# Performance work log

Measured on AMD Instinct MI355X. Metric: run time of the kernel, lower is better.

The kernel has to match this reference:

```python
import jax, jax.numpy as jnp
import numpy as np
import math

T, B, C, H, W = 1, 64, 512, 8, 8
E, NH, MEM, FF = 512, 8, 32, 2048
HD = E // NH            # 64 per-head channels
TOT = HD * H * W        # 4096 = flattened per-head dim (channels x spatial)


def conv2d(x, w, b):
    # NCHW conv with 'same' padding, matching torch.nn.Conv2d(padding='same')
    y = jax.lax.conv_general_dilated(x, w, (1, 1), 'SAME',
                                     dimension_numbers=('NCHW', 'OIHW', 'NCHW'))
    return y + b[None, :, None, None]


def layernorm(x, w, b, eps=1e-5):
    # LayerNorm over (C,H,W) with elementwise affine, matching nn.LayerNorm((C,H,W))
    m = jnp.mean(x, axis=(1, 2, 3), keepdims=True)
    v = jnp.var(x, axis=(1, 2, 3), keepdims=True)
    return (x - m) * jax.lax.rsqrt(v + eps) * w[None] + b[None]


def setup_inputs() -> dict:
    key = jax.random.key(0)
    ks = jax.random.split(key, 16)
    s = 0.02
    inp = {
        'input': jax.random.normal(ks[0], (T, B, C, H, W), jnp.float32),
        'attn_mask': jax.random.randint(ks[1], (B * NH, T, MEM), 0, 2) == 1,
        'concat_k': jax.random.normal(ks[2], (B, MEM, NH, TOT), jnp.float32),
        'concat_v': jax.random.normal(ks[3], (B, MEM, NH, TOT), jnp.float32),
        'proj_w': jax.random.normal(ks[4], (3 * E, C, 3, 3), jnp.float32) * s,
        'proj_b': jnp.zeros((3 * E,), jnp.float32),
        'out_w': jax.random.normal(ks[5], (E, E, 3, 3), jnp.float32) * s,
        'out_b': jnp.zeros((E,), jnp.float32),
        'lin1_w': jax.random.normal(ks[6], (FF, E, 3, 3), jnp.float32) * s,
        'lin1_b': jnp.zeros((FF,), jnp.float32),
        'lin2_w': jax.random.normal(ks[7], (E, FF, 3, 3), jnp.float32) * s,
        'lin2_b': jnp.zeros((E,), jnp.float32),
        'n1_w': jnp.ones((E, H, W), jnp.float32),
        'n1_b': jnp.zeros((E, H, W), jnp.float32),
        'n2_w': jnp.ones((E, H, W), jnp.float32),
        'n2_b': jnp.zeros((E, H, W), jnp.float32),
        'pos_w': jax.random.normal(ks[8], (MEM, H * W * E), jnp.float32) * s,
        'pos_b': jax.random.uniform(ks[9], (MEM, NH), jnp.float32, -0.1, 0.1),
    }
    return inp


def reference(input, attn_mask, concat_k, concat_v, proj_w, proj_b, out_w, out_b,
              lin1_w, lin1_b, lin2_w, lin2_b, n1_w, n1_b, n2_w, n2_b, pos_w, pos_b):
    x = input.reshape(T * B, C, H, W)
    kqv = conv2d(x, proj_w, proj_b)                      # [B, 3E, H, W]
    k0, q0, v0 = kqv[:, :E], kqv[:, E:2 * E], kqv[:, 2 * E:]

    def split_heads(t):  # [T*B,E,H,W] -> [B*NH, T, TOT]
        return t.reshape(T, B * NH, HD, H, W).transpose(1, 0, 2, 3, 4).reshape(B * NH, T, TOT)

    k, q, v = split_heads(k0), split_heads(q0), split_heads(v0)
    q = q / math.sqrt(TOT)

    def mem_pre(c):  # [B,MEM,NH,TOT] -> [B*NH, MEM-1, TOT]
        return c[:, 1:].transpose(1, 0, 2, 3).reshape(MEM - 1, B * NH, TOT).transpose(1, 0, 2)

    k = jnp.concatenate([mem_pre(concat_k), k], axis=1)  # [B*NH, MEM, TOT]
    v = jnp.concatenate([mem_pre(concat_v), v], axis=1)

    # learned relative-position bias on keys and logits
    pw = jnp.broadcast_to(pos_w[:, None, :], (MEM, B, NH * TOT)).reshape(MEM, B * NH, TOT).transpose(1, 0, 2)
    pb = jnp.broadcast_to(pos_b[:, None, :], (MEM, B, NH)).reshape(MEM, B * NH).transpose(1, 0)
    k = k + pw

    mask = jnp.where(attn_mask, -jnp.inf, 0.0).astype(q.dtype)
    mask = mask.at[:, :, -1].set(5.0)                    # current step always attendable (+5 bias)
    logits = mask + jnp.einsum('bqd,bkd->bqk', q, k) + pb[:, None, :]
    w_attn = jax.nn.softmax(logits, axis=-1)             # [B*NH, T, MEM]
    attn = jnp.einsum('bqk,bkd->bqd', w_attn, v)         # [B*NH, T, TOT]
    attn = attn.transpose(1, 0, 2).reshape(B, E, H, W)

    out = conv2d(attn, out_w, out_b)
    ret_k = k.transpose(1, 0, 2).reshape(MEM, B, NH, TOT).transpose(1, 0, 2, 3)
    ret_v = v.transpose(1, 0, 2).reshape(MEM, B, NH, TOT).transpose(1, 0, 2, 3)

    # norm_first=False path
    out = out + x[:, :E]
    out = layernorm(out, n1_w, n1_b)
    ff = conv2d(jax.nn.relu(conv2d(out, lin1_w, lin1_b)), lin2_w, lin2_b)
    out = layernorm(out + ff, n2_w, n2_b)
    return (out[None], ret_k, ret_v)
```

## Files before the change

kernel.cpp:

```cpp
#include <hip/hip_runtime.h>
#include <hip/hip_bf16.h>
#include <stdint.h>

typedef __attribute__((ext_vector_type(8))) short bf16x8;
typedef __attribute__((ext_vector_type(4))) float f32x4;

static __device__ __forceinline__ unsigned short f2bf(float f) {
  union { float f; unsigned int u; } v; v.f = f;
  unsigned int u = v.u;
  return (unsigned short)((u + 0x7FFFu + ((u >> 16) & 1u)) >> 16);
}

static __device__ __forceinline__ void gld16(const void* g, void* l) {
  __builtin_amdgcn_global_load_lds(
      (const __attribute__((address_space(1))) unsigned int*)g,
      (__attribute__((address_space(3))) unsigned int*)l, 16, 0, 0);
}

__global__ __launch_bounds__(256) void k_zero(uint4* __restrict__ p, int n) {
  int i = blockIdx.x * 256 + threadIdx.x;
  if (i < n) p[i] = make_uint4(0u, 0u, 0u, 0u);
}

__global__ __launch_bounds__(256) void k_wcvt(const float* __restrict__ in,
                                              unsigned short* __restrict__ out, int C) {
  int o = blockIdx.x, c0 = blockIdx.y << 9;
  int t = threadIdx.x;
  __shared__ float l[4608];
  const float* src = in + ((size_t)o * C + c0) * 9;
  for (int j = t; j < 4608; j += 256) l[j] = src[j];
  __syncthreads();
  unsigned short* dst = out + (size_t)o * 9 * C;
#pragma unroll
  for (int j = 0; j < 18; ++j) {
    int f = t * 18 + j;
    int tap = f >> 9, c = f & 511;
    dst[(size_t)tap * C + c0 + c] = f2bf(l[c * 9 + tap]);
  }
}

__global__ __launch_bounds__(256) void k_x2pad(const float* __restrict__ x,
                                               unsigned short* __restrict__ xp) {
  int b = blockIdx.x >> 3, c0 = (blockIdx.x & 7) << 6;
  int t = threadIdx.x;
  __shared__ float l[64][65];
  int cr = t >> 2, p0 = (t & 3) << 4;
  const float* src = x + ((size_t)b * 512 + c0 + cr) * 64 + p0;
#pragma unroll
  for (int j = 0; j < 4; ++j) {
    float4 v = *(const float4*)(src + j * 4);
    l[cr][p0 + j * 4 + 0] = v.x; l[cr][p0 + j * 4 + 1] = v.y;
    l[cr][p0 + j * 4 + 2] = v.z; l[cr][p0 + j * 4 + 3] = v.w;
  }
  __syncthreads();
  int pix = t >> 2, cc0 = (t & 3) << 4;
  size_t prow = (size_t)b * 100 + 11 + (pix >> 3) * 10 + (pix & 7);
  unsigned short pk[16];
#pragma unroll
  for (int j = 0; j < 16; ++j) pk[j] = f2bf(l[cc0 + j][pix]);
  *(uint4*)(xp + prow * 512 + c0 + cc0) = *(const uint4*)pk;
  *(uint4*)(xp + prow * 512 + c0 + cc0 + 8) = *(const uint4*)(pk + 8);
}

template <int EPI>
__global__ __launch_bounds__(256, 2) void k_gemm9(
    const unsigned short* __restrict__ Wt, int ldK,
    const unsigned short* __restrict__ Xp, int C, int tlog,
    int kiter, const float* __restrict__ bias,
    void* __restrict__ outv, int Cout, size_t zstride) {
  __shared__ unsigned short lds[2][2][8192];
  int t = threadIdx.x, lane = t & 63, wid = t >> 6;

  int gx = gridDim.x;
  int f = blockIdx.x + blockIdx.y * gx;
  int cpx = (gx * gridDim.y) >> 3;
  int fs = (f & 7) * cpx + (f >> 3);
  int bx = fs % gx, by = fs / gx;

  int O0 = bx << 7, M0 = by << 7;
  int kbase = blockIdx.z * kiter;
  int srow = lane >> 3, skg = (lane & 7) << 3;

  int wrow[4], pbv[4];
#pragma unroll
  for (int i = 0; i < 4; ++i) {
    int rl = wid * 8 + i * 32 + srow;
    wrow[i] = O0 + rl;
    int m = M0 + rl, b = m >> 6, pix = m & 63;
    pbv[i] = b * 100 + (pix >> 3) * 10 + (pix & 7);
  }

  f32x4 acc[4][4];
#pragma unroll
  for (int i = 0; i < 4; ++i)
#pragma unroll
    for (int j = 0; j < 4; ++j) acc[i][j] = (f32x4){0.f, 0.f, 0.f, 0.f};

  auto stage = [&](int buf, int kt) {
    int gk = kbase + kt;
    int tap = gk >> tlog;
    int c0 = (gk - (tap << tlog)) << 6;
    int toff = tap + 7 * ((tap * 11) >> 5);
#pragma unroll
    for (int i = 0; i < 4; ++i) {
      gld16(Wt + (size_t)wrow[i] * ldK + (gk << 6) + skg,
            &lds[buf][0][(wid * 8 + i * 32) * 64]);
      gld16(Xp + (size_t)(pbv[i] + toff) * C + c0 + skg,
            &lds[buf][1][(wid * 8 + i * 32) * 64]);
    }
  };

  int wr = wid >> 1, wc = wid & 1;
  int frow = lane & 15, fkb = (lane >> 4) << 3;

  auto compute = [&](int buf) {
    const unsigned short* Wl = &lds[buf][0][0];
    const unsigned short* Xl = &lds[buf][1][0];
#pragma unroll
    for (int kk = 0; kk < 2; ++kk) {
      bf16x8 af[4], bfv[4];
#pragma unroll
      for (int ff = 0; ff < 4; ++ff) {
        af[ff]  = *(const bf16x8*)(Wl + ((wr * 64 + ff * 16 + frow) << 6) + kk * 32 + fkb);
        bfv[ff] = *(const bf16x8*)(Xl + ((wc * 64 + ff * 16 + frow) << 6) + kk * 32 + fkb);
      }
#pragma unroll
      for (int fi = 0; fi < 4; ++fi)
#pragma unroll
        for (int fj = 0; fj < 4; ++fj)
          acc[fi][fj] = __builtin_amdgcn_mfma_f32_16x16x32_bf16(af[fi], bfv[fj], acc[fi][fj], 0, 0, 0);
    }
  };

  stage(0, 0);
  __syncthreads();
  for (int kt = 0; kt < kiter; ++kt) {
    int cur = kt & 1;
    if (kt + 1 < kiter) stage(cur ^ 1, kt + 1);
    compute(cur);
    __syncthreads();
  }

  int ob = O0 + wr * 64, mb = M0 + wc * 64;
  int r0 = (lane >> 4) << 2, cm = lane & 15;
  if (EPI == 4) {
    unsigned short* outp = (unsigned short*)outv;
#pragma unroll
    for (int fi = 0; fi < 4; ++fi) {
      int oo = ob + fi * 16 + r0;
      float4 bv = *(const float4*)(bias + oo);
#pragma unroll
      for (int fj = 0; fj < 4; ++fj) {
        int mm = mb + fj * 16 + cm;
        int bb = mm >> 6, pix = mm & 63;
        size_t prow = (size_t)bb * 100 + 11 + (pix >> 3) * 10 + (pix & 7);
        unsigned short pk[4];
        pk[0] = f2bf(fmaxf(acc[fi][fj][0] + bv.x, 0.f));
        pk[1] = f2bf(fmaxf(acc[fi][fj][1] + bv.y, 0.f));
        pk[2] = f2bf(fmaxf(acc[fi][fj][2] + bv.z, 0.f));
        pk[3] = f2bf(fmaxf(acc[fi][fj][3] + bv.w, 0.f));
        *(ushort4*)(outp + prow * Cout + oo) = *(const ushort4*)pk;
      }
    }
  } else {
    float* out = (float*)outv + (size_t)blockIdx.z * zstride;
#pragma unroll
    for (int fi = 0; fi < 4; ++fi) {
#pragma unroll
      for (int fj = 0; fj < 4; ++fj) {
        int mm = mb + fj * 16 + cm;
        int bb = mm >> 6, pix = mm & 63;
#pragma unroll
        for (int r = 0; r < 4; ++r) {
          int oo = ob + fi * 16 + r0 + r;
          float v = acc[fi][fj][r];
          if (EPI == 0) v += bias[oo];
          out[((size_t)bb * Cout + oo) * 64 + pix] = v;
        }
      }
    }
  }
}

__global__ __launch_bounds__(256) void k_sum2(const float* __restrict__ a,
                                              const float* __restrict__ b,
                                              const float* __restrict__ bias,
                                              float* __restrict__ o) {
  int i = (blockIdx.x * 256 + threadIdx.x) * 4;
  int ch = (i >> 6) % 1536;
  float4 va = *(const float4*)(a + i);
  float4 vb = *(const float4*)(b + i);
  float bs = bias[ch];
  *(float4*)(o + i) = make_float4(va.x + vb.x + bs, va.y + vb.y + bs,
                                  va.z + vb.z + bs, va.w + vb.w + bs);
}

__global__ __launch_bounds__(256) void k_attnK(
    const float* __restrict__ kqv, const float* __restrict__ ck,
    const float* __restrict__ pw, const float* __restrict__ pb,
    float* __restrict__ rk, float* __restrict__ logits) {
  int idx = blockIdx.x;
  int h = idx & 7, m = (idx >> 3) & 31, b = idx >> 8;
  int t = threadIdx.x, lane = t & 63, wid = t >> 6;
  int i0 = t << 4;
  int hd = i0 >> 6, pix = i0 & 63;

  const float* src = (m < 31)
      ? (ck + (((size_t)(b * 32 + m + 1) * 8 + h) << 12) + i0)
      : (kqv + ((size_t)(b * 1536 + h * 64 + hd) << 6) + pix);
  const float* qs = kqv + ((size_t)(b * 1536 + 512 + h * 64 + hd) << 6) + pix;
  const float* pws = pw + ((size_t)m << 15) + (h << 12) + i0;
  float* dst = rk + (((size_t)(b * 32 + m) * 8 + h) << 12) + i0;

  float part = 0.f;
#pragma unroll
  for (int j = 0; j < 4; ++j) {
    float4 a = *(const float4*)(src + j * 4);
    float4 p = *(const float4*)(pws + j * 4);
    float4 q = *(const float4*)(qs + j * 4);
    float4 kk;
    kk.x = a.x + p.x; kk.y = a.y + p.y; kk.z = a.z + p.z; kk.w = a.w + p.w;
    *(float4*)(dst + j * 4) = kk;
    part += 0.015625f * (q.x * kk.x + q.y * kk.y + q.z * kk.z + q.w * kk.w);
  }
#pragma unroll
  for (int s = 32; s; s >>= 1) part += __shfl_xor(part, s);
  __shared__ float red[4];
  if (lane == 0) red[wid] = part;
  __syncthreads();
  if (t == 0)
    logits[((b << 3) + h) * 32 + m] = red[0] + red[1] + red[2] + red[3] + pb[m * 8 + h];
}

__global__ __launch_bounds__(256) void k_attnV(
    const float* __restrict__ kqv, const int* __restrict__ mask,
    const float* __restrict__ cv, const float* __restrict__ logits,
    float* __restrict__ rv, float* __restrict__ attnb) {
  int bh = blockIdx.x, b = bh >> 3, h = bh & 7;
  int t = threadIdx.x;
  int d = (blockIdx.y << 10) + (t << 2);
  int hd = d >> 6, pix = d & 63;

  float lg[32];
#pragma unroll
  for (int j = 0; j < 8; ++j) {
    float4 v = *(const float4*)(logits + bh * 32 + j * 4);
    lg[j * 4 + 0] = v.x; lg[j * 4 + 1] = v.y; lg[j * 4 + 2] = v.z; lg[j * 4 + 3] = v.w;
  }
  float mx = -INFINITY;
#pragma unroll
  for (int m = 0; m < 32; ++m) {
    if (m == 31) lg[m] += 5.0f;
    else if (mask[bh * 32 + m] != 0) lg[m] = -INFINITY;
    mx = fmaxf(mx, lg[m]);
  }
  float sm = 0.f;
#pragma unroll
  for (int m = 0; m < 32; ++m) { lg[m] = __expf(lg[m] - mx); sm += lg[m]; }
  float rs = 1.f / sm;

  float4 acc = make_float4(0.f, 0.f, 0.f, 0.f);
  for (int m = 0; m < 32; ++m) {
    const float* src = (m < 31)
        ? (cv + (((size_t)(b * 32 + m + 1) * 8 + h) << 12) + d)
        : (kqv + ((size_t)(b * 1536 + 1024 + h * 64 + hd) << 6) + pix);
    float4 v = *(const float4*)src;
    *(float4*)(rv + (((size_t)(b * 32 + m) * 8 + h) << 12) + d) = v;
    float wm = lg[m] * rs;
    acc.x += wm * v.x; acc.y += wm * v.y; acc.z += wm * v.z; acc.w += wm * v.w;
  }
  *(float4*)(attnb + ((size_t)(b * 512 + h * 64 + hd) << 6) + pix) = acc;
}

__global__ __launch_bounds__(256) void k_lnfuse4(
    const float* __restrict__ p0, const float* __restrict__ p1,
    const float* __restrict__ p2, const float* __restrict__ p3,
    const float* __restrict__ resid, const float* __restrict__ bias,
    const float* __restrict__ w, const float* __restrict__ beta,
    float* __restrict__ out) {
  int bb = blockIdx.x, t = threadIdx.x, lane = t & 63, wid = t >> 6;
  size_t base = (size_t)bb << 15;
  float s = 0.f, sq = 0.f;
  for (int i = t * 4; i < 32768; i += 1024) {
    float4 v0 = *(const float4*)(p0 + base + i);
    float4 v1 = *(const float4*)(p1 + base + i);
    float4 v2 = *(const float4*)(p2 + base + i);
    float4 v3 = *(const float4*)(p3 + base + i);
    float4 vr = *(const float4*)(resid + base + i);
    float bs = bias[i >> 6];
    float x0 = v0.x + v1.x + v2.x + v3.x + vr.x + bs;
    float x1 = v0.y + v1.y + v2.y + v3.y + vr.y + bs;
    float x2 = v0.z + v1.z + v2.z + v3.z + vr.z + bs;
    float x3 = v0.w + v1.w + v2.w + v3.w + vr.w + bs;
    s += x0 + x1 + x2 + x3;
    sq += x0 * x0 + x1 * x1 + x2 * x2 + x3 * x3;
  }
#pragma unroll
  for (int k = 32; k; k >>= 1) { s += __shfl_xor(s, k); sq += __shfl_xor(sq, k); }
  __shared__ float rsm[4], rqm[4];
  if (lane == 0) { rsm[wid] = s; rqm[wid] = sq; }
  __syncthreads();
  s = rsm[0] + rsm[1] + rsm[2] + rsm[3];
  sq = rqm[0] + rqm[1] + rqm[2] + rqm[3];
  float mean = s * (1.f / 32768.f);
  float var = sq * (1.f / 32768.f) - mean * mean;
  float rinv = rsqrtf(var + 1e-5f);
  for (int i = t * 4; i < 32768; i += 1024) {
    float4 v0 = *(const float4*)(p0 + base + i);
    float4 v1 = *(const float4*)(p1 + base + i);
    float4 v2 = *(const float4*)(p2 + base + i);
    float4 v3 = *(const float4*)(p3 + base + i);
    float4 vr = *(const float4*)(resid + base + i);
    float bs = bias[i >> 6];
    float4 vw = *(const float4*)(w + i);
    float4 vt = *(const float4*)(beta + i);
    float4 r;
    r.x = (v0.x + v1.x + v2.x + v3.x + vr.x + bs - mean) * rinv * vw.x + vt.x;
    r.y = (v0.y + v1.y + v2.y + v3.y + vr.y + bs - mean) * rinv * vw.y + vt.y;
    r.z = (v0.z + v1.z + v2.z + v3.z + vr.z + bs - mean) * rinv * vw.z + vt.z;
    r.w = (v0.w + v1.w + v2.w + v3.w + vr.w + bs - mean) * rinv * vw.w + vt.w;
    *(float4*)(out + base + i) = r;
  }
}

extern "C" void kernel_launch(void* const* d_in, const int* in_sizes, int n_in,
                              void* d_out, int out_size, void* d_ws, size_t ws_size,
                              hipStream_t stream) {
  const float* x     = (const float*)d_in[0];
  const int*   mask  = (const int*)d_in[1];
  const float* ck    = (const float*)d_in[2];
  const float* cv    = (const float*)d_in[3];
  const float* projw = (const float*)d_in[4];
  const float* projb = (const float*)d_in[5];
  const float* outw  = (const float*)d_in[6];
  const float* outb  = (const float*)d_in[7];
  const float* l1w   = (const float*)d_in[8];
  const float* l1b   = (const float*)d_in[9];
  const float* l2w   = (const float*)d_in[10];
  const float* l2b   = (const float*)d_in[11];
  const float* n1w   = (const float*)d_in[12];
  const float* n1b   = (const float*)d_in[13];
  const float* n2w   = (const float*)d_in[14];
  const float* n2b   = (const float*)d_in[15];
  const float* posw  = (const float*)d_in[16];
  const float* posb  = (const float*)d_in[17];

  char* ws = (char*)d_ws;
  unsigned short* wbP   = (unsigned short*)(ws);
  unsigned short* wbO   = (unsigned short*)(ws + 14155776);
  unsigned short* wbL1  = (unsigned short*)(ws + 18874368);
  unsigned short* wbL2  = (unsigned short*)(ws + 37748736);
  unsigned short* xpadI = (unsigned short*)(ws + 56623104);
  unsigned short* apad  = (unsigned short*)(ws + 63176704);
  unsigned short* l1pad = (unsigned short*)(ws + 69730304);
  unsigned short* ffpad = (unsigned short*)(ws + 76283904);
  float* kqvA   = (float*)(ws + 102498304);
  float* kqvB   = (float*)(ws + 127664128);
  float* kqv    = (float*)(ws + 152829952);
  float* logits = (float*)(ws + 177995776);
  float* res    = (float*)(ws + 178061312);
  float* ln1    = (float*)(ws + 211615744);
  float* attnb  = (float*)(ws + 220004352);

  float* out0 = (float*)d_out;
  float* rk = out0 + 2097152;
  float* rv = rk + 67108864;

  k_zero<<<11200, 256, 0, stream>>>((uint4*)(ws + 56623104), 2867200);

  k_wcvt<<<dim3(1536, 1), 256, 0, stream>>>(projw, wbP, 512);
  k_wcvt<<<dim3(512, 1), 256, 0, stream>>>(outw, wbO, 512);
  k_wcvt<<<dim3(2048, 1), 256, 0, stream>>>(l1w, wbL1, 512);
  k_wcvt<<<dim3(512, 4), 256, 0, stream>>>(l2w, wbL2, 2048);

  k_x2pad<<<512, 256, 0, stream>>>(x, xpadI);

  k_gemm9<3><<<dim3(12, 32, 2), 256, 0, stream>>>(wbP, 4608, xpadI, 512, 3, 36, nullptr, kqvA, 1536, 25165824 / 4);
  k_sum2<<<6144, 256, 0, stream>>>(kqvA, kqvB, projb, kqv);

  k_attnK<<<16384, 256, 0, stream>>>(kqv, ck, posw, posb, rk, logits);
  k_attnV<<<dim3(512, 4), 256, 0, stream>>>(kqv, mask, cv, logits, rv, attnb);
  k_x2pad<<<512, 256, 0, stream>>>(attnb, apad);

  k_gemm9<3><<<dim3(4, 32, 4), 256, 0, stream>>>(wbO, 4608, apad, 512, 3, 18, nullptr, res, 512, 2097152);
  k_lnfuse4<<<64, 256, 0, stream>>>(res, res + 2097152, res + 4194304, res + 6291456,
                                    x, outb, n1w, n1b, ln1);
  k_x2pad<<<512, 256, 0, stream>>>(ln1, l1pad);

  k_gemm9<4><<<dim3(16, 32, 1), 256, 0, stream>>>(wbL1, 4608, l1pad, 512, 3, 72, l1b, ffpad, 2048, 0);

  k_gemm9<3><<<dim3(4, 32, 4), 256, 0, stream>>>(wbL2, 18432, ffpad, 2048, 5, 72, nullptr, res, 512, 2097152);
  k_lnfuse4<<<64, 256, 0, stream>>>(res, res + 2097152, res + 4194304, res + 6291456,
                                    ln1, l2b, n2w, n2b, out0);
}
```

Before: 845.9 us.

## Overlap ret_k/ret_v memory copies with conv GEMMs via extra copy blocks

The bulk copying of concat_k+pos_w into ret_k and concat_v into ret_v for the 31 past memory slots moves out of the attention kernels. It now runs on extra blocks prepended to the projection and lin1 GEMM launches, so this bandwidth-bound work can overlap compute-bound MFMA work. The projection GEMM also drops its split-K-by-2 plus separate sum kernel and writes bias-added output directly. The grids become 1D with manual decoding of z. The risk is that copy blocks compete for CUs and bandwidth with GEMM tiles, and that the unsplit projection has fewer blocks.

Result: slower. 881.4 us (+4.2%).

```diff
diff --git a/kernel.cpp b/kernel.cpp
--- a/kernel.cpp
+++ b/kernel.cpp
@@ -67,18 +67,49 @@
     const unsigned short* __restrict__ Wt, int ldK,
     const unsigned short* __restrict__ Xp, int C, int tlog,
     int kiter, const float* __restrict__ bias,
-    void* __restrict__ outv, int Cout, size_t zstride) {
+    void* __restrict__ outv, int Cout, size_t zstride,
+    int gx, int nxy, int NS,
+    const float* __restrict__ s_src, const float* __restrict__ s_pw,
+    float* __restrict__ s_dst) {
+  int t = threadIdx.x;
+  if (blockIdx.x < NS) {
+    for (int u = blockIdx.x; u < 15872; u += NS) {
+      int b = u / 248;
+      int rem = u - b * 248;
+      int m = rem >> 3, h = rem & 7;
+      const float* src = s_src + (((size_t)(b * 32 + m + 1) * 8 + h) << 12);
+      float* dst = s_dst + (((size_t)(b * 32 + m) * 8 + h) << 12);
+      if (s_pw) {
+        const float* pws = s_pw + ((size_t)m << 15) + (h << 12);
+#pragma unroll
+        for (int j = 0; j < 4; ++j) {
+          int i = t * 4 + j * 1024;
+          float4 a = *(const float4*)(src + i);
+          float4 p = *(const float4*)(pws + i);
+          *(float4*)(dst + i) = make_float4(a.x + p.x, a.y + p.y, a.z + p.z, a.w + p.w);
+        }
+      } else {
+#pragma unroll
+        for (int j = 0; j < 4; ++j) {
+          int i = t * 4 + j * 1024;
+          *(float4*)(dst + i) = *(const float4*)(src + i);
+        }
+      }
+    }
+    return;
+  }
+
   __shared__ unsigned short lds[2][2][8192];
-  int t = threadIdx.x, lane = t & 63, wid = t >> 6;
-
-  int gx = gridDim.x;
-  int f = blockIdx.x + blockIdx.y * gx;
-  int cpx = (gx * gridDim.y) >> 3;
+  int lane = t & 63, wid = t >> 6;
+  int id = blockIdx.x - NS;
+  int bz = id / nxy;
+  int f = id - bz * nxy;
+  int cpx = nxy >> 3;
   int fs = (f & 7) * cpx + (f >> 3);
   int bx = fs % gx, by = fs / gx;
 
   int O0 = bx << 7, M0 = by << 7;
-  int kbase = blockIdx.z * kiter;
+  int kbase = bz * kiter;
   int srow = lane >> 3, skg = (lane & 7) << 3;
 
   int wrow[4], pbv[4];
@@ -163,7 +194,7 @@
       }
     }
   } else {
-    float* out = (float*)outv + (size_t)blockIdx.z * zstride;
+    float* out = (float*)outv + (size_t)bz * zstride;
 #pragma unroll
     for (int fi = 0; fi < 4; ++fi) {
 #pragma unroll
@@ -180,19 +211,6 @@
       }
     }
   }
-}
-
-__global__ __launch_bounds__(256) void k_sum2(const float* __restrict__ a,
-                                              const float* __restrict__ b,
-                                              const float* __restrict__ bias,
-                                              float* __restrict__ o) {
-  int i = (blockIdx.x * 256 + threadIdx.x) * 4;
-  int ch = (i >> 6) % 1536;
-  float4 va = *(const float4*)(a + i);
-  float4 vb = *(const float4*)(b + i);
-  float bs = bias[ch];
-  *(float4*)(o + i) = make_float4(va.x + vb.x + bs, va.y + vb.y + bs,
-                                  va.z + vb.z + bs, va.w + vb.w + bs);
 }
 
 __global__ __launch_bounds__(256) void k_attnK(
@@ -210,18 +228,21 @@
       : (kqv + ((size_t)(b * 1536 + h * 64 + hd) << 6) + pix);
   const float* qs = kqv + ((size_t)(b * 1536 + 512 + h * 64 + hd) << 6) + pix;
   const float* pws = pw + ((size_t)m << 15) + (h << 12) + i0;
-  float* dst = rk + (((size_t)(b * 32 + m) * 8 + h) << 12) + i0;
 
   float part = 0.f;
+  float4 kk[4];
 #pragma unroll
   for (int j = 0; j < 4; ++j) {
     float4 a = *(const float4*)(src + j * 4);
     float4 p = *(const float4*)(pws + j * 4);
     float4 q = *(const float4*)(qs + j * 4);
-    float4 kk;
-    kk.x = a.x + p.x; kk.y = a.y + p.y; kk.z = a.z + p.z; kk.w = a.w + p.w;
-    *(float4*)(dst + j * 4) = kk;
-    part += 0.015625f * (q.x * kk.x + q.y * kk.y + q.z * kk.z + q.w * kk.w);
+    kk[j].x = a.x + p.x; kk[j].y = a.y + p.y; kk[j].z = a.z + p.z; kk[j].w = a.w + p.w;
+    part += 0.015625f * (q.x * kk[j].x + q.y * kk[j].y + q.z * kk[j].z + q.w * kk[j].w);
+  }
+  if (m == 31) {
+    float* dst = rk + (((size_t)(b * 32 + 31) * 8 + h) << 12) + i0;
+#pragma unroll
+    for (int j = 0; j < 4; ++j) *(float4*)(dst + j * 4) = kk[j];
   }
 #pragma unroll
   for (int s = 32; s; s >>= 1) part += __shfl_xor(part, s);
@@ -260,13 +281,16 @@
   float rs = 1.f / sm;
 
   float4 acc = make_float4(0.f, 0.f, 0.f, 0.f);
-  for (int m = 0; m < 32; ++m) {
-    const float* src = (m < 31)
-        ? (cv + (((size_t)(b * 32 + m + 1) * 8 + h) << 12) + d)
-        : (kqv + ((size_t)(b * 1536 + 1024 + h * 64 + hd) << 6) + pix);
+  for (int m = 0; m < 31; ++m) {
+    const float* src = cv + (((size_t)(b * 32 + m + 1) * 8 + h) << 12) + d;
     float4 v = *(const float4*)src;
-    *(float4*)(rv + (((size_t)(b * 32 + m) * 8 + h) << 12) + d) = v;
     float wm = lg[m] * rs;
+    acc.x += wm * v.x; acc.y += wm * v.y; acc.z += wm * v.z; acc.w += wm * v.w;
+  }
+  {
+    float4 v = *(const float4*)(kqv + ((size_t)(b * 1536 + 1024 + h * 64 + hd) << 6) + pix);
+    *(float4*)(rv + (((size_t)(b * 32 + 31) * 8 + h) << 12) + d) = v;
+    float wm = lg[31] * rs;
     acc.x += wm * v.x; acc.y += wm * v.y; acc.z += wm * v.z; acc.w += wm * v.w;
   }
   *(float4*)(attnb + ((size_t)(b * 512 + h * 64 + hd) << 6) + pix) = acc;
@@ -354,13 +378,11 @@
   unsigned short* apad  = (unsigned short*)(ws + 63176704);
   unsigned short* l1pad = (unsigned short*)(ws + 69730304);
   unsigned short* ffpad = (unsigned short*)(ws + 76283904);
-  float* kqvA   = (float*)(ws + 102498304);
-  float* kqvB   = (float*)(ws + 127664128);
-  float* kqv    = (float*)(ws + 152829952);
-  float* logits = (float*)(ws + 177995776);
-  float* res    = (float*)(ws + 178061312);
-  float* ln1    = (float*)(ws + 211615744);
-  float* attnb  = (float*)(ws + 220004352);
+  float* kqv    = (float*)(ws + 102498304);
+  float* logits = (float*)(ws + 127664128);
+  float* res    = (float*)(ws + 127729664);
+  float* ln1    = (float*)(ws + 161284096);
+  float* attnb  = (float*)(ws + 169672704);
 
   float* out0 = (float*)d_out;
   float* rk = out0 + 2097152;
@@ -375,21 +397,24 @@
 
   k_x2pad<<<512, 256, 0, stream>>>(x, xpadI);
 
-  k_gemm9<3><<<dim3(12, 32, 2), 256, 0, stream>>>(wbP, 4608, xpadI, 512, 3, 36, nullptr, kqvA, 1536, 25165824 / 4);
-  k_sum2<<<6144, 256, 0, stream>>>(kqvA, kqvB, projb, kqv);
+  k_gemm9<0><<<640, 256, 0, stream>>>(wbP, 4608, xpadI, 512, 3, 72, projb, kqv, 1536, 0,
+                                      12, 384, 256, cv, nullptr, rv);
 
   k_attnK<<<16384, 256, 0, stream>>>(kqv, ck, posw, posb, rk, logits);
   k_attnV<<<dim3(512, 4), 256, 0, stream>>>(kqv, mask, cv, logits, rv, attnb);
   k_x2pad<<<512, 256, 0, stream>>>(attnb, apad);
 
-  k_gemm9<3><<<dim3(4, 32, 4), 256, 0, stream>>>(wbO, 4608, apad, 512, 3, 18, nullptr, res, 512, 2097152);
+  k_gemm9<3><<<512, 256, 0, stream>>>(wbO, 4608, apad, 512, 3, 18, nullptr, res, 512, 2097152,
+                                      4, 128, 0, nullptr, nullptr, nullptr);
   k_lnfuse4<<<64, 256, 0, stream>>>(res, res + 2097152, res + 4194304, res + 6291456,
                                     x, outb, n1w, n1b, ln1);
   k_x2pad<<<512, 256, 0, stream>>>(ln1, l1pad);
 
-  k_gemm9<4><<<dim3(16, 32, 1), 256, 0, stream>>>(wbL1, 4608, l1pad, 512, 3, 72, l1b, ffpad, 2048, 0);
-
-  k_gemm9<3><<<dim3(4, 32, 4), 256, 0, stream>>>(wbL2, 18432, ffpad, 2048, 5, 72, nullptr, res, 512, 2097152);
+  k_gemm9<4><<<768, 256, 0, stream>>>(wbL1, 4608, l1pad, 512, 3, 72, l1b, ffpad, 2048, 0,
+                                      16, 512, 256, ck, posw, rk);
+
+  k_gemm9<3><<<512, 256, 0, stream>>>(wbL2, 18432, ffpad, 2048, 5, 72, nullptr, res, 512, 2097152,
+                                      4, 128, 0, nullptr, nullptr, nullptr);
   k_lnfuse4<<<64, 256, 0, stream>>>(res, res + 2097152, res + 4194304, res + 6291456,
                                     ln1, l2b, n2w, n2b, out0);
 }
```

## Merge weight/input prep kernels and split layernorm into parallel stat/apply passes

Applied to the files above, without the earlier changes.

Merges the four weight-conversion launches and the input padding launch into a single k_prep kernel that dispatches on block index, cutting launch overhead. Replaces the 64-block fused layernorm, which used only one block per sample, with a 512-block stats kernel that writes the summed pre-norm tensor and per-segment partial sums, plus a 512-block apply kernel. This spreads the layernorm work across far more CUs. The cost is an extra intermediate buffer write and read and one additional launch per layernorm.

After: 750.3 us. 1.13x faster.

```diff
diff --git a/kernel.cpp b/kernel.cpp
--- a/kernel.cpp
+++ b/kernel.cpp
@@ -22,20 +22,51 @@
   if (i < n) p[i] = make_uint4(0u, 0u, 0u, 0u);
 }
 
-__global__ __launch_bounds__(256) void k_wcvt(const float* __restrict__ in,
-                                              unsigned short* __restrict__ out, int C) {
-  int o = blockIdx.x, c0 = blockIdx.y << 9;
-  int t = threadIdx.x;
+__global__ __launch_bounds__(256) void k_prep(
+    const float* __restrict__ projw, const float* __restrict__ outw,
+    const float* __restrict__ l1w, const float* __restrict__ l2w,
+    const float* __restrict__ x,
+    unsigned short* __restrict__ wbP, unsigned short* __restrict__ wbO,
+    unsigned short* __restrict__ wbL1, unsigned short* __restrict__ wbL2,
+    unsigned short* __restrict__ xp) {
   __shared__ float l[4608];
-  const float* src = in + ((size_t)o * C + c0) * 9;
-  for (int j = t; j < 4608; j += 256) l[j] = src[j];
-  __syncthreads();
-  unsigned short* dst = out + (size_t)o * 9 * C;
-#pragma unroll
-  for (int j = 0; j < 18; ++j) {
-    int f = t * 18 + j;
-    int tap = f >> 9, c = f & 511;
-    dst[(size_t)tap * C + c0 + c] = f2bf(l[c * 9 + tap]);
+  int bid = blockIdx.x, t = threadIdx.x;
+  if (bid < 6144) {
+    const float* in; unsigned short* out; int o, C, c0;
+    if (bid < 1536)      { in = projw; out = wbP;  o = bid;               C = 512;  c0 = 0; }
+    else if (bid < 2048) { in = outw;  out = wbO;  o = bid - 1536;        C = 512;  c0 = 0; }
+    else if (bid < 4096) { in = l1w;   out = wbL1; o = bid - 2048;        C = 512;  c0 = 0; }
+    else                 { in = l2w;   out = wbL2; o = (bid - 4096) >> 2; C = 2048; c0 = ((bid - 4096) & 3) << 9; }
+    const float* src = in + ((size_t)o * C + c0) * 9;
+    for (int j = t; j < 4608; j += 256) l[j] = src[j];
+    __syncthreads();
+    unsigned short* dst = out + (size_t)o * 9 * C;
+#pragma unroll
+    for (int j = 0; j < 18; ++j) {
+      int f = t * 18 + j;
+      int tap = f >> 9, c = f & 511;
+      dst[(size_t)tap * C + c0 + c] = f2bf(l[c * 9 + tap]);
+    }
+  } else {
+    int idx = bid - 6144;
+    int b = idx >> 3, c0 = (idx & 7) << 6;
+    float (*lt)[65] = (float(*)[65])l;
+    int cr = t >> 2, p0 = (t & 3) << 4;
+    const float* src = x + ((size_t)b * 512 + c0 + cr) * 64 + p0;
+#pragma unroll
+    for (int j = 0; j < 4; ++j) {
+      float4 v = *(const float4*)(src + j * 4);
+      lt[cr][p0 + j * 4 + 0] = v.x; lt[cr][p0 + j * 4 + 1] = v.y;
+      lt[cr][p0 + j * 4 + 2] = v.z; lt[cr][p0 + j * 4 + 3] = v.w;
+    }
+    __syncthreads();
+    int pix = t >> 2, cc0 = (t & 3) << 4;
+    size_t prow = (size_t)b * 100 + 11 + (pix >> 3) * 10 + (pix & 7);
+    unsigned short pk[16];
+#pragma unroll
+    for (int j = 0; j < 16; ++j) pk[j] = f2bf(lt[cc0 + j][pix]);
+    *(uint4*)(xp + prow * 512 + c0 + cc0) = *(const uint4*)pk;
+    *(uint4*)(xp + prow * 512 + c0 + cc0 + 8) = *(const uint4*)(pk + 8);
   }
 }
 
@@ -272,53 +303,68 @@
   *(float4*)(attnb + ((size_t)(b * 512 + h * 64 + hd) << 6) + pix) = acc;
 }
 
-__global__ __launch_bounds__(256) void k_lnfuse4(
-    const float* __restrict__ p0, const float* __restrict__ p1,
-    const float* __restrict__ p2, const float* __restrict__ p3,
-    const float* __restrict__ resid, const float* __restrict__ bias,
-    const float* __restrict__ w, const float* __restrict__ beta,
-    float* __restrict__ out) {
-  int bb = blockIdx.x, t = threadIdx.x, lane = t & 63, wid = t >> 6;
+__global__ __launch_bounds__(256) void k_lnstat(
+    const float* __restrict__ p, const float* __restrict__ resid,
+    const float* __restrict__ bias, float* __restrict__ xbuf,
+    float2* __restrict__ stat) {
+  int bb = blockIdx.x, seg = blockIdx.y, t = threadIdx.x;
+  int lane = t & 63, wid = t >> 6;
   size_t base = (size_t)bb << 15;
   float s = 0.f, sq = 0.f;
-  for (int i = t * 4; i < 32768; i += 1024) {
-    float4 v0 = *(const float4*)(p0 + base + i);
-    float4 v1 = *(const float4*)(p1 + base + i);
-    float4 v2 = *(const float4*)(p2 + base + i);
-    float4 v3 = *(const float4*)(p3 + base + i);
+#pragma unroll
+  for (int j = 0; j < 4; ++j) {
+    int i = (seg << 12) + t * 4 + j * 1024;
+    float4 v0 = *(const float4*)(p + base + i);
+    float4 v1 = *(const float4*)(p + 2097152 + base + i);
+    float4 v2 = *(const float4*)(p + 4194304 + base + i);
+    float4 v3 = *(const float4*)(p + 6291456 + base + i);
     float4 vr = *(const float4*)(resid + base + i);
     float bs = bias[i >> 6];
-    float x0 = v0.x + v1.x + v2.x + v3.x + vr.x + bs;
-    float x1 = v0.y + v1.y + v2.y + v3.y + vr.y + bs;
-    float x2 = v0.z + v1.z + v2.z + v3.z + vr.z + bs;
-    float x3 = v0.w + v1.w + v2.w + v3.w + vr.w + bs;
-    s += x0 + x1 + x2 + x3;
-    sq += x0 * x0 + x1 * x1 + x2 * x2 + x3 * x3;
+    float4 xx;
+    xx.x = v0.x + v1.x + v2.x + v3.x + vr.x + bs;
+    xx.y = v0.y + v1.y + v2.y + v3.y + vr.y + bs;
+    xx.z = v0.z + v1.z + v2.z + v3.z + vr.z + bs;
+    xx.w = v0.w + v1.w + v2.w + v3.w + vr.w + bs;
+    *(float4*)(xbuf + base + i) = xx;
+    s += xx.x + xx.y + xx.z + xx.w;
+    sq += xx.x * xx.x + xx.y * xx.y + xx.z * xx.z + xx.w * xx.w;
   }
 #pragma unroll
   for (int k = 32; k; k >>= 1) { s += __shfl_xor(s, k); sq += __shfl_xor(sq, k); }
   __shared__ float rsm[4], rqm[4];
   if (lane == 0) { rsm[wid] = s; rqm[wid] = sq; }
   __syncthreads();
-  s = rsm[0] + rsm[1] + rsm[2] + rsm[3];
-  sq = rqm[0] + rqm[1] + rqm[2] + rqm[3];
+  if (t == 0)
+    stat[bb * 8 + seg] = make_float2(rsm[0] + rsm[1] + rsm[2] + rsm[3],
+                                     rqm[0] + rqm[1] + rqm[2] + rqm[3]);
+}
+
+__global__ __launch_bounds__(256) void k_lnapply(
+    const float* __restrict__ xbuf, const float2* __restrict__ stat,
+    const float* __restrict__ w, const float* __restrict__ beta,
+    float* __restrict__ out) {
+  int bb = blockIdx.x, seg = blockIdx.y, t = threadIdx.x;
+  size_t base = (size_t)bb << 15;
+  float s = 0.f, sq = 0.f;
+#pragma unroll
+  for (int k = 0; k < 8; ++k) {
+    float2 st = stat[bb * 8 + k];
+    s += st.x; sq += st.y;
+  }
   float mean = s * (1.f / 32768.f);
   float var = sq * (1.f / 32768.f) - mean * mean;
   float rinv = rsqrtf(var + 1e-5f);
-  for (int i = t * 4; i < 32768; i += 1024) {
-    float4 v0 = *(const float4*)(p0 + base + i);
-    float4 v1 = *(const float4*)(p1 + base + i);
-    float4 v2 = *(const float4*)(p2 + base + i);
-    float4 v3 = *(const float4*)(p3 + base + i);
-    float4 vr = *(const float4*)(resid + base + i);
-    float bs = bias[i >> 6];
+#pragma unroll
+  for (int j = 0; j < 4; ++j) {
+    int i = (seg << 12) + t * 4 + j * 1024;
+    float4 xx = *(const float4*)(xbuf + base + i);
     float4 vw = *(const float4*)(w + i);
     float4 vt = *(const float4*)(beta + i);
     float4 r;
-    r.x = (v0.x + v1.x + v2.x + v3.x + vr.x + bs - mean) * rinv * vw.x + vt.x;
-    r.y = (v0.y + v1.y + v2.y + v3.y + vr.y + bs - mean) * rinv * vw.y + vt.y;
-    r.z = (v0.z + v1.z + v2.z + v3.z + vr.z + bs - mean) * rinv * vw.z + vt.z;
-    r.w = (v0.w + v1.w + v2.w + v3.w + vr.w + bs - mean) * rinv * vw.w + vt.w;
+    r.x = (xx.x - mean) * rinv * vw.x + vt.x;
+    r.y = (xx.y - mean) * rinv * vw.y + vt.y;
+    r.z = (xx.z - mean) * rinv * vw.z + vt.z;
+    r.w = (xx.w - mean) * rinv * vw.w + vt.w;
     *(float4*)(out + base + i) = r;
   }
 }
@@ -361,6 +407,10 @@
   float* res    = (float*)(ws + 178061312);
   float* ln1    = (float*)(ws + 211615744);
   float* attnb  = (float*)(ws + 220004352);
+  float* xbuf1  = (float*)(ws + 228392960);
+  float* xbuf2  = (float*)(ws + 236781568);
+  float2* stat1 = (float2*)(ws + 245170176);
+  float2* stat2 = (float2*)(ws + 245174272);
 
   float* out0 = (float*)d_out;
   float* rk = out0 + 2097152;
@@ -368,14 +418,9 @@
 
   k_zero<<<11200, 256, 0, stream>>>((uint4*)(ws + 56623104), 2867200);
 
-  k_wcvt<<<dim3(1536, 1), 256, 0, stream>>>(projw, wbP, 512);
-  k_wcvt<<<dim3(512, 1), 256, 0, stream>>>(outw, wbO, 512);
-  k_wcvt<<<dim3(2048, 1), 256, 0, stream>>>(l1w, wbL1, 512);
-  k_wcvt<<<dim3(512, 4), 256, 0, stream>>>(l2w, wbL2, 2048);
-
-  k_x2pad<<<512, 256, 0, stream>>>(x, xpadI);
-
-  k_gemm9<3><<<dim3(12, 32, 2), 256, 0, stream>>>(wbP, 4608, xpadI, 512, 3, 36, nullptr, kqvA, 1536, 25165824 / 4);
+  k_prep<<<6656, 256, 0, stream>>>(projw, outw, l1w, l2w, x, wbP, wbO, wbL1, wbL2, xpadI);
+
+  k_gemm9<3><<<dim3(12, 32, 2), 256, 0, stream>>>(wbP, 4608, xpadI, 512, 3, 36, nullptr, kqvA, 1536, 6291456);
   k_sum2<<<6144, 256, 0, stream>>>(kqvA, kqvB, projb, kqv);
 
   k_attnK<<<16384, 256, 0, stream>>>(kqv, ck, posw, posb, rk, logits);
@@ -383,13 +428,13 @@
   k_x2pad<<<512, 256, 0, stream>>>(attnb, apad);
 
   k_gemm9<3><<<dim3(4, 32, 4), 256, 0, stream>>>(wbO, 4608, apad, 512, 3, 18, nullptr, res, 512, 2097152);
-  k_lnfuse4<<<64, 256, 0, stream>>>(res, res + 2097152, res + 4194304, res + 6291456,
-                                    x, outb, n1w, n1b, ln1);
+  k_lnstat<<<dim3(64, 8), 256, 0, stream>>>(res, x, outb, xbuf1, stat1);
+  k_lnapply<<<dim3(64, 8), 256, 0, stream>>>(xbuf1, stat1, n1w, n1b, ln1);
   k_x2pad<<<512, 256, 0, stream>>>(ln1, l1pad);
 
   k_gemm9<4><<<dim3(16, 32, 1), 256, 0, stream>>>(wbL1, 4608, l1pad, 512, 3, 72, l1b, ffpad, 2048, 0);
 
   k_gemm9<3><<<dim3(4, 32, 4), 256, 0, stream>>>(wbL2, 18432, ffpad, 2048, 5, 72, nullptr, res, 512, 2097152);
-  k_lnfuse4<<<64, 256, 0, stream>>>(res, res + 2097152, res + 4194304, res + 6291456,
-                                    ln1, l2b, n2w, n2b, out0);
-}
+  k_lnstat<<<dim3(64, 8), 256, 0, stream>>>(res, ln1, l2b, xbuf2, stat2);
+  k_lnapply<<<dim3(64, 8), 256, 0, stream>>>(xbuf2, stat2, n2w, n2b, out0);
+}
```
